# Kernel tuning notes

Measured on AMD Instinct MI355X. Metric: run time of the kernel, lower is better.

The kernel has to match this reference:

```python
import jax, jax.numpy as jnp
import numpy as np

VOCAB = 100000
EMB = 100
HID = 100
CTX_LEN = 60          # must equal MAX_DESC_LEN for linear_1 to fit
FACT_LEN = 20
DESC_LEN = 60


def setup_inputs() -> dict:
    key = jax.random.key(0)
    ks = jax.random.split(key, 12)
    s = 0.05
    context = jax.random.randint(ks[0], (CTX_LEN, FACT_LEN), 1, VOCAB)
    fact_lengths = jax.random.randint(ks[1], (CTX_LEN,), 1, FACT_LEN)
    description = jax.random.randint(ks[2], (DESC_LEN,), 1, VOCAB)
    emb_ctx = jax.random.normal(ks[3], (VOCAB, EMB), jnp.float32) * s
    emb_ctx = emb_ctx.at[0].set(0.0)  # padding_idx=0
    emb_dec = jax.random.normal(ks[4], (VOCAB, EMB), jnp.float32) * s
    emb_dec = emb_dec.at[0].set(0.0)
    w1 = jax.random.normal(ks[5], (HID, CTX_LEN * HID), jnp.float32) * s
    b1 = jax.random.normal(ks[6], (HID,), jnp.float32) * s
    w_ih = jax.random.normal(ks[7], (3 * HID, EMB), jnp.float32) * s
    w_hh = jax.random.normal(ks[8], (3 * HID, HID), jnp.float32) * s
    b_ih = jax.random.normal(ks[9], (3 * HID,), jnp.float32) * s
    b_hh = jax.random.normal(ks[10], (3 * HID,), jnp.float32) * s
    w_out = jax.random.normal(ks[11], (VOCAB, HID), jnp.float32) * s
    b_out = jnp.zeros((VOCAB,), jnp.float32)
    return {"context": context, "fact_lengths": fact_lengths, "description": description,
            "emb_ctx": emb_ctx, "emb_dec": emb_dec, "w1": w1, "b1": b1,
            "w_ih": w_ih, "w_hh": w_hh, "b_ih": b_ih, "b_hh": b_hh,
            "w_out": w_out, "b_out": b_out}


def _forward(context, description, emb_ctx, emb_dec, w1, b1,
             w_ih, w_hh, b_ih, b_hh, w_out, b_out):
    # ---- InputModule: embed + positional fact encoder ----
    emb = emb_ctx[context]                       # [CTX_LEN, FACT_LEN, EMB]
    slen, elen = FACT_LEN, EMB
    s = jnp.arange(slen, dtype=jnp.float32) / (slen - 1)   # [slen]
    e = jnp.arange(elen, dtype=jnp.float32) / (elen - 1)   # [elen]
    l = 1.0 - s[:, None] - e[None, :] * (1.0 - 2.0 * s[:, None])  # [slen, elen]
    facts = jnp.sum(emb * l[None], axis=1)       # [CTX_LEN, EMB]

    # ---- initial decoder hidden from flattened facts ----
    h0 = facts.reshape(1, -1) @ w1.T + b1        # [1, HID]

    x0 = emb_dec[1][None, :]                     # SOS token embedding [1, EMB]

    def step(carry, tok):
        h, x = carry
        gi = x @ w_ih.T + b_ih                   # [1, 3H]
        gh = h @ w_hh.T + b_hh
        i_r, i_z, i_n = jnp.split(gi, 3, axis=-1)
        h_r, h_z, h_n = jnp.split(gh, 3, axis=-1)
        r = jax.nn.sigmoid(i_r + h_r)
        z = jax.nn.sigmoid(i_z + h_z)
        n = jnp.tanh(i_n + r * h_n)
        h_new = (1.0 - z) * n + z * h            # [1, HID]
        logits = h_new @ w_out.T + b_out         # [1, VOCAB]
        logp = jax.nn.log_softmax(logits, axis=-1)
        loss_t = -logp[0, tok]                   # NLLLoss, batch 1
        x_next = emb_dec[tok][None, :]           # teacher forcing
        return (h_new, x_next), loss_t

    (_, _), losses = jax.lax.scan(step, (h0, x0), description)
    return jnp.sum(losses).reshape(1)            # matches torch FloatTensor([.])


def reference(context, fact_lengths, description, emb_ctx, emb_dec, w1, b1,
              w_ih, w_hh, b_ih, b_hh, w_out, b_out):
    # fact_lengths is unused by the original forward (PositionalFactEncoder ignores it)
    return _forward(context, description, emb_ctx, emb_dec, w1, b1,
                    w_ih, w_hh, b_ih, b_hh, w_out, b_out)
```

## Files before the change

### kernel.cpp

```cpp
#include <hip/hip_runtime.h>
#include <hip/hip_bf16.h>
#include <math.h>

#define VOCAB 100000
#define EMB 100
#define HID 100
#define CTX_LEN 60
#define FACT_LEN 20
#define DESC_LEN 60
#define NCHUNK (VOCAB / 16)

#define WS_FACTS 0
#define WS_X     6000
#define WS_H0    12000
#define WS_GI    12160
#define WS_H     30160
#define WS_MS    36864

typedef __attribute__((ext_vector_type(8))) short short8;
typedef __attribute__((ext_vector_type(4))) float f32x4;

static __device__ __forceinline__ unsigned short f2bf(float f) {
    union { float f; unsigned u; } x; x.f = f;
    unsigned r = (x.u + 0x7FFFu + ((x.u >> 16) & 1u)) >> 16;
    return (unsigned short)r;
}

__global__ __launch_bounds__(128) void k1_prep(const int* __restrict__ context,
                                               const int* __restrict__ desc,
                                               const float* __restrict__ emb_ctx,
                                               const float* __restrict__ emb_dec,
                                               float* __restrict__ ws,
                                               float* __restrict__ out) {
    int b = blockIdx.x, tid = threadIdx.x;
    if (b < 60) {
        __shared__ int toks[20];
        if (tid < 20) toks[tid] = context[b * 20 + tid];
        __syncthreads();
        if (tid < 100) {
            float ef = tid * (1.f / 99.f);
            float acc = 0.f;
            #pragma unroll
            for (int s = 0; s < 20; s++) {
                float sf = s * (1.f / 19.f);
                float l = 1.f - sf - ef * (1.f - 2.f * sf);
                acc = fmaf(emb_ctx[toks[s] * 100 + tid], l, acc);
            }
            ws[WS_FACTS + b * 100 + tid] = acc;
        }
    } else {
        int t = b - 60;
        int tok = (t == 0) ? 1 : desc[t - 1];
        if (tid < 100) ws[WS_X + t * 100 + tid] = emb_dec[tok * 100 + tid];
        if (b == 60 && tid == 0) out[0] = 0.f;
    }
}

__global__ __launch_bounds__(320) void k2_h0_gi(const float* __restrict__ w1,
                                                const float* __restrict__ b1,
                                                const float* __restrict__ w_ih,
                                                const float* __restrict__ b_ih,
                                                float* __restrict__ ws) {
    int b = blockIdx.x, tid = threadIdx.x;
    if (b < 100) {
        __shared__ float red[320];
        const float* facts = ws + WS_FACTS;
        const float* wr = w1 + b * 6000;
        float p = 0.f;
        for (int k = tid; k < 6000; k += 320) p = fmaf(facts[k], wr[k], p);
        red[tid] = p; __syncthreads();
        if (tid < 64) red[tid] += red[256 + tid];
        __syncthreads();
        for (int st = 128; st > 0; st >>= 1) {
            if (tid < st) red[tid] += red[tid + st];
            __syncthreads();
        }
        if (tid == 0) ws[WS_H0 + b] = red[0] + b1[b];
    } else {
        int t = b - 100;
        __shared__ float xs[100];
        if (tid < 100) xs[tid] = ws[WS_X + t * 100 + tid];
        __syncthreads();
        if (tid < 300) {
            float p = b_ih[tid];
            const float* wr = w_ih + tid * 100;
            #pragma unroll 4
            for (int k = 0; k < 100; k++) p = fmaf(wr[k], xs[k], p);
            ws[WS_GI + t * 300 + tid] = p;
        }
    }
}

__global__ __launch_bounds__(320, 1) void k3_gru(const float* __restrict__ w_hh,
                                                 const float* __restrict__ b_hh,
                                                 float* __restrict__ ws) {
    __shared__ __align__(16) float gi_lds[18000];
    __shared__ __align__(16) float h_hist[6000];
    __shared__ __align__(16) unsigned short h_bf[128];

    const int tid = threadIdx.x;
    const int wave = tid >> 6, lane = tid & 63;
    const int q = lane >> 4, n = lane & 15;
    const int l = lane;
    const int j = 20 * wave + l;

    short8 bfr[16];
    #pragma unroll
    for (int i = 0; i < 4; i++) {
        int row;
        if (i == 0)      row = 20 * wave + n;
        else if (i == 1) row = 100 + 20 * wave + n;
        else if (i == 2) row = 200 + 20 * wave + n;
        else {
            if (n < 4)       row = 20 * wave + 16 + n;
            else if (n < 8)  row = 100 + 20 * wave + 12 + n;
            else if (n < 12) row = 200 + 20 * wave + 8 + n;
            else             row = -1;
        }
        const float* wr = w_hh + (row < 0 ? 0 : row) * 100;
        #pragma unroll
        for (int kt = 0; kt < 4; kt++) {
            int k0 = kt * 32 + q * 8;
            float va[8];
            #pragma unroll
            for (int jj = 0; jj < 8; jj++) va[jj] = 0.f;
            if (row >= 0) {
                if (k0 + 4 <= 100) {
                    float4 a = *(const float4*)(wr + k0);
                    va[0] = a.x; va[1] = a.y; va[2] = a.z; va[3] = a.w;
                }
                if (k0 + 8 <= 100) {
                    float4 b = *(const float4*)(wr + k0 + 4);
                    va[4] = b.x; va[5] = b.y; va[6] = b.z; va[7] = b.w;
                }
            }
            short8 f;
            #pragma unroll
            for (int jj = 0; jj < 8; jj++) f[jj] = (short)f2bf(va[jj]);
            bfr[i * 4 + kt] = f;
        }
    }

    {
        const float4* g4 = (const float4*)(ws + WS_GI);
        float4* l4 = (float4*)gi_lds;
        for (int k = tid; k < 4500; k += 320) l4[k] = g4[k];
    }

    float hreg = 0.f, bh0 = 0.f, bh1 = 0.f, bh2 = 0.f;
    if (l < 20) {
        hreg = ws[WS_H0 + j];
        bh0 = b_hh[j]; bh1 = b_hh[100 + j]; bh2 = b_hh[200 + j];
        h_bf[j] = f2bf(hreg);
    }
    if (tid >= 100 && tid < 128) h_bf[tid] = 0;
    __syncthreads();

    const int s_lo  = (l < 16) ? l : 0;
    const int s3r   = (l < 16) ? 0 : (l - 16);
    const int s3z   = (l < 16) ? 4 : (l - 12);
    const int s3n   = (l < 16) ? 8 : (l - 8);

    for (int t = 0; t < 60; t++) {
        short8 afr[4];
        #pragma unroll
        for (int kt = 0; kt < 4; kt++)
            afr[kt] = *(const short8*)&h_bf[kt * 32 + q * 8];

        float val[4];
        #pragma unroll
        for (int i = 0; i < 4; i++) {
            f32x4 z4 = {0.f, 0.f, 0.f, 0.f};
            f32x4 a01 = __builtin_amdgcn_mfma_f32_16x16x32_bf16(afr[0], bfr[i * 4 + 0], z4, 0, 0, 0);
            a01 = __builtin_amdgcn_mfma_f32_16x16x32_bf16(afr[1], bfr[i * 4 + 1], a01, 0, 0, 0);
            f32x4 a23 = __builtin_amdgcn_mfma_f32_16x16x32_bf16(afr[2], bfr[i * 4 + 2], z4, 0, 0, 0);
            a23 = __builtin_amdgcn_mfma_f32_16x16x32_bf16(afr[3], bfr[i * 4 + 3], a23, 0, 0, 0);
            val[i] = a01[0] + a23[0];
        }

        float v0  = __shfl(val[0], s_lo, 64);
        float v1  = __shfl(val[1], s_lo, 64);
        float v2  = __shfl(val[2], s_lo, 64);
        float w3r = __shfl(val[3], s3r, 64);
        float w3z = __shfl(val[3], s3z, 64);
        float w3n = __shfl(val[3], s3n, 64);

        if (l < 20) {
            float ghr = ((l < 16) ? v0 : w3r) + bh0;
            float ghz = ((l < 16) ? v1 : w3z) + bh1;
            float ghn = ((l < 16) ? v2 : w3n) + bh2;
            float gir = gi_lds[t * 300 + j];
            float giz = gi_lds[t * 300 + 100 + j];
            float gin = gi_lds[t * 300 + 200 + j];
            float r = 1.f / (1.f + __expf(-(gir + ghr)));
            float z = 1.f / (1.f + __expf(-(giz + ghz)));
            float a = fmaf(r, ghn, gin);
            float tt = __expf(-2.f * fabsf(a));
            float nn = copysignf((1.f - tt) / (1.f + tt), a);
            hreg = (1.f - z) * nn + z * hreg;
            h_bf[j] = f2bf(hreg);
            h_hist[t * 100 + j] = hreg;
        }
        __syncthreads();
    }

    {
        float4* Hg = (float4*)(ws + WS_H);
        const float4* h4 = (const float4*)h_hist;
        for (int k = tid; k < 1500; k += 320) Hg[k] = h4[k];
    }
}

__global__ __launch_bounds__(256, 1) void k4_logits(const float* __restrict__ w_out,
                                                    const float* __restrict__ b_out,
                                                    float* __restrict__ ws,
                                                    int nwaves) {
    const float* H = ws + WS_H;
    float* ms = ws + WS_MS;
    const int lane = threadIdx.x & 63;
    const int gw = blockIdx.x * 4 + (threadIdx.x >> 6);
    const int q = lane >> 4, n = lane & 15;
    const int k_base = q * 8;

    short8 afr[4][4];
    #pragma unroll
    for (int mt = 0; mt < 4; mt++) {
        int m = mt * 16 + n;
        #pragma unroll
        for (int kt = 0; kt < 4; kt++) {
            int k0 = kt * 32 + k_base;
            float va[8];
            #pragma unroll
            for (int jj = 0; jj < 8; jj++) va[jj] = 0.f;
            if (m < 60) {
                if (k0 + 4 <= 100) {
                    float4 a = *(const float4*)(H + m * 100 + k0);
                    va[0] = a.x; va[1] = a.y; va[2] = a.z; va[3] = a.w;
                }
                if (k0 + 8 <= 100) {
                    float4 b = *(const float4*)(H + m * 100 + k0 + 4);
                    va[4] = b.x; va[5] = b.y; va[6] = b.z; va[7] = b.w;
                }
            }
            short8 f;
            #pragma unroll
            for (int jj = 0; jj < 8; jj++) f[jj] = (short)f2bf(va[jj]);
            afr[mt][kt] = f;
        }
    }

    float mS[16], sS[16];
    #pragma unroll
    for (int i = 0; i < 16; i++) { mS[i] = -3.0e38f; sS[i] = 0.f; }

    for (int c = gw; c < NCHUNK; c += nwaves) {
        int row = c * 16 + n;
        short8 bfr[4];
        #pragma unroll
        for (int kt = 0; kt < 4; kt++) {
            int k0 = kt * 32 + k_base;
            float va[8];
            #pragma unroll
            for (int jj = 0; jj < 8; jj++) va[jj] = 0.f;
            if (k0 + 4 <= 100) {
                float4 a = *(const float4*)(w_out + row * 100 + k0);
                va[0] = a.x; va[1] = a.y; va[2] = a.z; va[3] = a.w;
            }
            if (k0 + 8 <= 100) {
                float4 b = *(const float4*)(w_out + row * 100 + k0 + 4);
                va[4] = b.x; va[5] = b.y; va[6] = b.z; va[7] = b.w;
            }
            short8 f;
            #pragma unroll
            for (int jj = 0; jj < 8; jj++) f[jj] = (short)f2bf(va[jj]);
            bfr[kt] = f;
        }
        float bo = b_out[row];
        #pragma unroll
        for (int mt = 0; mt < 4; mt++) {
            f32x4 acc = {0.f, 0.f, 0.f, 0.f};
            acc = __builtin_amdgcn_mfma_f32_16x16x32_bf16(afr[mt][0], bfr[0], acc, 0, 0, 0);
            acc = __builtin_amdgcn_mfma_f32_16x16x32_bf16(afr[mt][1], bfr[1], acc, 0, 0, 0);
            acc = __builtin_amdgcn_mfma_f32_16x16x32_bf16(afr[mt][2], bfr[2], acc, 0, 0, 0);
            acc = __builtin_amdgcn_mfma_f32_16x16x32_bf16(afr[mt][3], bfr[3], acc, 0, 0, 0);
            #pragma unroll
            for (int reg = 0; reg < 4; reg++) {
                float x = acc[reg] + bo;
                int i = mt * 4 + reg;
                float mo = mS[i];
                float mn = fmaxf(mo, x);
                sS[i] = sS[i] * __expf(mo - mn) + __expf(x - mn);
                mS[i] = mn;
            }
        }
    }

    #pragma unroll
    for (int i = 0; i < 16; i++) {
        float m = mS[i], s = sS[i];
        #pragma unroll
        for (int off = 1; off < 16; off <<= 1) {
            float m2 = __shfl_xor(m, off);
            float s2 = __shfl_xor(s, off);
            float mn = fmaxf(m, m2);
            s = s * __expf(m - mn) + s2 * __expf(m2 - mn);
            m = mn;
        }
        mS[i] = m; sS[i] = s;
    }
    if (n == 0) {
        #pragma unroll
        for (int mt = 0; mt < 4; mt++) {
            #pragma unroll
            for (int reg = 0; reg < 4; reg++) {
                int t = mt * 16 + q * 4 + reg;
                int i = mt * 4 + reg;
                if (t < 60) {
                    float2 val; val.x = mS[i]; val.y = sS[i];
                    ((float2*)ms)[t * nwaves + gw] = val;
                }
            }
        }
    }
}

__global__ __launch_bounds__(256) void k5_final(const int* __restrict__ desc,
                                                const float* __restrict__ w_out,
                                                const float* __restrict__ b_out,
                                                const float* __restrict__ ws,
                                                float* __restrict__ out,
                                                int nwaves) {
    int t = blockIdx.x, tid = threadIdx.x;
    __shared__ float sm[256], ss[256], sd[256];
    const float2* ms = (const float2*)(ws + WS_MS);
    float m = -3.0e38f, s = 0.f;
    for (int i = tid; i < nwaves; i += 256) {
        float2 p = ms[t * nwaves + i];
        float mn = fmaxf(m, p.x);
        s = s * __expf(m - mn) + p.y * __expf(p.x - mn);
        m = mn;
    }
    sm[tid] = m; ss[tid] = s; __syncthreads();
    for (int st = 128; st > 0; st >>= 1) {
        if (tid < st) {
            float mo = sm[tid], so = ss[tid];
            float m2 = sm[tid + st], s2 = ss[tid + st];
            float mn = fmaxf(mo, m2);
            sm[tid] = mn;
            ss[tid] = so * __expf(mo - mn) + s2 * __expf(m2 - mn);
        }
        __syncthreads();
    }
    int tok = desc[t];
    float p = 0.f;
    if (tid < 100) p = ws[WS_H + t * 100 + tid] * w_out[tok * 100 + tid];
    sd[tid] = p; __syncthreads();
    for (int st = 128; st > 0; st >>= 1) {
        if (tid < st) sd[tid] += sd[tid + st];
        __syncthreads();
    }
    if (tid == 0) {
        float logit = sd[0] + b_out[tok];
        float loss = sm[0] + logf(ss[0]) - logit;
        atomicAdd(out, loss);
    }
}

extern "C" void kernel_launch(void* const* d_in, const int* in_sizes, int n_in,
                              void* d_out, int out_size, void* d_ws, size_t ws_size,
                              hipStream_t stream) {
    const int*   context = (const int*)d_in[0];
    const int*   desc    = (const int*)d_in[2];
    const float* emb_ctx = (const float*)d_in[3];
    const float* emb_dec = (const float*)d_in[4];
    const float* w1      = (const float*)d_in[5];
    const float* b1      = (const float*)d_in[6];
    const float* w_ih    = (const float*)d_in[7];
    const float* w_hh    = (const float*)d_in[8];
    const float* b_ih    = (const float*)d_in[9];
    const float* b_hh    = (const float*)d_in[10];
    const float* w_out   = (const float*)d_in[11];
    const float* b_out   = (const float*)d_in[12];
    float* out = (float*)d_out;
    float* ws  = (float*)d_ws;

    int nblocks = 1024;
    size_t need = (size_t)(WS_MS + 60 * (nblocks * 4) * 2) * 4;
    if (ws_size < need) nblocks = 256;
    int nwaves = nblocks * 4;

    k1_prep  <<<120, 128, 0, stream>>>(context, desc, emb_ctx, emb_dec, ws, out);
    k2_h0_gi <<<160, 320, 0, stream>>>(w1, b1, w_ih, b_ih, ws);
    k3_gru   <<<1,   320, 0, stream>>>(w_hh, b_hh, ws);
    k4_logits<<<nblocks, 256, 0, stream>>>(w_out, b_out, ws, nwaves);
    k5_final <<<60,  256, 0, stream>>>(desc, w_out, b_out, ws, out, nwaves);
}
```

Before: 214.4 us.

## Pre-convert w_out to padded bf16 in idle blocks alongside the serial GRU

The single-block GRU kernel is launched with 255 extra blocks that convert w_out from fp32 into a bf16 copy padded to 128 columns in the workspace. This uses the otherwise idle compute units during the serial recurrence. The logits kernel then loads ready-made bf16 fragments with plain vector loads, which removes the per-chunk conversion and reads fewer bytes. The cost is extra workspace traffic and memory that is written unconditionally, even when the workspace-size check falls back to fewer blocks. The extra blocks may also contend with the GRU block for memory bandwidth.

```diff
diff --git a/kernel.cpp b/kernel.cpp
--- a/kernel.cpp
+++ b/kernel.cpp
@@ -16,6 +16,7 @@
 #define WS_GI    12160
 #define WS_H     30160
 #define WS_MS    36864
+#define WS_WBF   1048576
 
 typedef __attribute__((ext_vector_type(8))) short short8;
 typedef __attribute__((ext_vector_type(4))) float f32x4;
@@ -91,9 +92,30 @@
     }
 }
 
-__global__ __launch_bounds__(320, 1) void k3_gru(const float* __restrict__ w_hh,
-                                                 const float* __restrict__ b_hh,
-                                                 float* __restrict__ ws) {
+__global__ __launch_bounds__(320, 1) void k3_gru_cvt(const float* __restrict__ w_hh,
+                                                     const float* __restrict__ b_hh,
+                                                     const float* __restrict__ w_out,
+                                                     float* __restrict__ ws) {
+    if (blockIdx.x != 0) {
+        const int bid = blockIdx.x - 1;
+        unsigned short* wbf = (unsigned short*)((char*)ws + WS_WBF * 4);
+        uint2* out4 = (uint2*)wbf;
+        const int total = VOCAB * 128 / 4;
+        const int stride = 255 * 320;
+        for (int i = bid * 320 + threadIdx.x; i < total; i += stride) {
+            int row = i >> 5;
+            int k0 = (i & 31) * 4;
+            uint2 r;
+            if (k0 + 4 <= 100) {
+                float4 v = *(const float4*)(w_out + row * 100 + k0);
+                r.x = (unsigned)f2bf(v.x) | ((unsigned)f2bf(v.y) << 16);
+                r.y = (unsigned)f2bf(v.z) | ((unsigned)f2bf(v.w) << 16);
+            } else { r.x = 0u; r.y = 0u; }
+            out4[i] = r;
+        }
+        return;
+    }
+
     __shared__ __align__(16) float gi_lds[18000];
     __shared__ __align__(16) float h_hist[6000];
     __shared__ __align__(16) unsigned short h_bf[128];
@@ -211,11 +233,11 @@
     }
 }
 
-__global__ __launch_bounds__(256, 1) void k4_logits(const float* __restrict__ w_out,
-                                                    const float* __restrict__ b_out,
+__global__ __launch_bounds__(256, 1) void k4_logits(const float* __restrict__ b_out,
                                                     float* __restrict__ ws,
                                                     int nwaves) {
     const float* H = ws + WS_H;
+    const unsigned short* wbf = (const unsigned short*)((const char*)ws + WS_WBF * 4);
     float* ms = ws + WS_MS;
     const int lane = threadIdx.x & 63;
     const int gw = blockIdx.x * 4 + (threadIdx.x >> 6);
@@ -255,26 +277,10 @@
 
     for (int c = gw; c < NCHUNK; c += nwaves) {
         int row = c * 16 + n;
+        const short8* bp = (const short8*)(wbf + (size_t)row * 128);
         short8 bfr[4];
         #pragma unroll
-        for (int kt = 0; kt < 4; kt++) {
-            int k0 = kt * 32 + k_base;
-            float va[8];
-            #pragma unroll
-            for (int jj = 0; jj < 8; jj++) va[jj] = 0.f;
-            if (k0 + 4 <= 100) {
-                float4 a = *(const float4*)(w_out + row * 100 + k0);
-                va[0] = a.x; va[1] = a.y; va[2] = a.z; va[3] = a.w;
-            }
-            if (k0 + 8 <= 100) {
-                float4 b = *(const float4*)(w_out + row * 100 + k0 + 4);
-                va[4] = b.x; va[5] = b.y; va[6] = b.z; va[7] = b.w;
-            }
-            short8 f;
-            #pragma unroll
-            for (int jj = 0; jj < 8; jj++) f[jj] = (short)f2bf(va[jj]);
-            bfr[kt] = f;
-        }
+        for (int kt = 0; kt < 4; kt++) bfr[kt] = bp[kt * 4 + q];
         float bo = b_out[row];
         #pragma unroll
         for (int mt = 0; mt < 4; mt++) {
@@ -385,13 +391,15 @@
     float* ws  = (float*)d_ws;
 
     int nblocks = 1024;
-    size_t need = (size_t)(WS_MS + 60 * (nblocks * 4) * 2) * 4;
+    size_t need = (size_t)(WS_WBF) * 4 + (size_t)VOCAB * 128 * 2;
+    size_t need_ms = (size_t)(WS_MS + 60 * (nblocks * 4) * 2) * 4;
+    if (need_ms > need) need = need_ms;
     if (ws_size < need) nblocks = 256;
     int nwaves = nblocks * 4;
 
-    k1_prep  <<<120, 128, 0, stream>>>(context, desc, emb_ctx, emb_dec, ws, out);
-    k2_h0_gi <<<160, 320, 0, stream>>>(w1, b1, w_ih, b_ih, ws);
-    k3_gru   <<<1,   320, 0, stream>>>(w_hh, b_hh, ws);
-    k4_logits<<<nblocks, 256, 0, stream>>>(w_out, b_out, ws, nwaves);
-    k5_final <<<60,  256, 0, stream>>>(desc, w_out, b_out, ws, out, nwaves);
-}
+    k1_prep   <<<120, 128, 0, stream>>>(context, desc, emb_ctx, emb_dec, ws, out);
+    k2_h0_gi  <<<160, 320, 0, stream>>>(w1, b1, w_ih, b_ih, ws);
+    k3_gru_cvt<<<256, 320, 0, stream>>>(w_hh, b_hh, w_out, ws);
+    k4_logits <<<nblocks, 256, 0, stream>>>(b_out, ws, nwaves);
+    k5_final  <<<60,  256, 0, stream>>>(desc, w_out, b_out, ws, out, nwaves);
+}
```

Result: no change. 211.5 us (-1.3%).

## Fuse fact encoding into h0 kernel and fix logits grid to 256 blocks

Applied to the files above, without the earlier changes.

Merges the prep and h0/input-gate kernels into one launch. Each h0 block now recomputes the positional fact encoding from embedding gathers, folded directly into its w1 dot product, and the decoder-input embedding is gathered inline in the gate blocks. This removes one kernel launch and the facts/x round-trip through the workspace, at the cost of redundant gathers and arithmetic in all 100 blocks. The logits kernel is also pinned to 256 blocks (1024 waves) as a compile-time constant, instead of picking 1024 blocks when the workspace allows. That gives each wave more vocab chunks and shrinks the partial-softmax reduction in the final kernel, in exchange for less parallelism in the logits GEMV.

```diff
diff --git a/kernel.cpp b/kernel.cpp
--- a/kernel.cpp
+++ b/kernel.cpp
@@ -9,9 +9,8 @@
 #define FACT_LEN 20
 #define DESC_LEN 60
 #define NCHUNK (VOCAB / 16)
-
-#define WS_FACTS 0
-#define WS_X     6000
+#define NWAVES 1024
+
 #define WS_H0    12000
 #define WS_GI    12160
 #define WS_H     30160
@@ -26,60 +25,57 @@
     return (unsigned short)r;
 }
 
-__global__ __launch_bounds__(128) void k1_prep(const int* __restrict__ context,
+__global__ __launch_bounds__(320) void k1_prep(const int* __restrict__ context,
                                                const int* __restrict__ desc,
                                                const float* __restrict__ emb_ctx,
                                                const float* __restrict__ emb_dec,
+                                               const float* __restrict__ w1,
+                                               const float* __restrict__ b1,
+                                               const float* __restrict__ w_ih,
+                                               const float* __restrict__ b_ih,
                                                float* __restrict__ ws,
                                                float* __restrict__ out) {
     int b = blockIdx.x, tid = threadIdx.x;
-    if (b < 60) {
-        __shared__ int toks[20];
-        if (tid < 20) toks[tid] = context[b * 20 + tid];
-        __syncthreads();
-        if (tid < 100) {
-            float ef = tid * (1.f / 99.f);
-            float acc = 0.f;
-            #pragma unroll
-            for (int s = 0; s < 20; s++) {
-                float sf = s * (1.f / 19.f);
-                float l = 1.f - sf - ef * (1.f - 2.f * sf);
-                acc = fmaf(emb_ctx[toks[s] * 100 + tid], l, acc);
-            }
-            ws[WS_FACTS + b * 100 + tid] = acc;
-        }
-    } else {
-        int t = b - 60;
-        int tok = (t == 0) ? 1 : desc[t - 1];
-        if (tid < 100) ws[WS_X + t * 100 + tid] = emb_dec[tok * 100 + tid];
-        if (b == 60 && tid == 0) out[0] = 0.f;
-    }
-}
-
-__global__ __launch_bounds__(320) void k2_h0_gi(const float* __restrict__ w1,
-                                                const float* __restrict__ b1,
-                                                const float* __restrict__ w_ih,
-                                                const float* __restrict__ b_ih,
-                                                float* __restrict__ ws) {
-    int b = blockIdx.x, tid = threadIdx.x;
     if (b < 100) {
+        __shared__ int toks[1200];
         __shared__ float red[320];
-        const float* facts = ws + WS_FACTS;
+        for (int i = tid; i < 1200; i += 320) toks[i] = context[i];
+        __syncthreads();
         const float* wr = w1 + b * 6000;
-        float p = 0.f;
-        for (int k = tid; k < 6000; k += 320) p = fmaf(facts[k], wr[k], p);
-        red[tid] = p; __syncthreads();
+        float acc = 0.f;
+        for (int p = tid; p < 1200; p += 320) {
+            int c = p / 20, s = p - c * 20;
+            const float* er = emb_ctx + (size_t)toks[p] * 100;
+            const float* wc = wr + c * 100;
+            float sf = s * (1.f / 19.f);
+            float l0 = 1.f - sf;
+            float l1 = 1.f - 2.f * sf;
+            float pacc = 0.f;
+            #pragma unroll 4
+            for (int e = 0; e < 100; e++) {
+                float l = fmaf(-(e * (1.f / 99.f)), l1, l0);
+                pacc = fmaf(er[e] * l, wc[e], pacc);
+            }
+            acc += pacc;
+        }
+        red[tid] = acc; __syncthreads();
         if (tid < 64) red[tid] += red[256 + tid];
         __syncthreads();
         for (int st = 128; st > 0; st >>= 1) {
             if (tid < st) red[tid] += red[tid + st];
             __syncthreads();
         }
-        if (tid == 0) ws[WS_H0 + b] = red[0] + b1[b];
+        if (tid == 0) {
+            ws[WS_H0 + b] = red[0] + b1[b];
+            if (b == 0) out[0] = 0.f;
+        }
     } else {
         int t = b - 100;
         __shared__ float xs[100];
-        if (tid < 100) xs[tid] = ws[WS_X + t * 100 + tid];
+        __shared__ int tok_s;
+        if (tid == 0) tok_s = (t == 0) ? 1 : desc[t - 1];
+        __syncthreads();
+        if (tid < 100) xs[tid] = emb_dec[tok_s * 100 + tid];
         __syncthreads();
         if (tid < 300) {
             float p = b_ih[tid];
@@ -213,8 +209,7 @@
 
 __global__ __launch_bounds__(256, 1) void k4_logits(const float* __restrict__ w_out,
                                                     const float* __restrict__ b_out,
-                                                    float* __restrict__ ws,
-                                                    int nwaves) {
+                                                    float* __restrict__ ws) {
     const float* H = ws + WS_H;
     float* ms = ws + WS_MS;
     const int lane = threadIdx.x & 63;
@@ -253,7 +248,7 @@
     #pragma unroll
     for (int i = 0; i < 16; i++) { mS[i] = -3.0e38f; sS[i] = 0.f; }
 
-    for (int c = gw; c < NCHUNK; c += nwaves) {
+    for (int c = gw; c < NCHUNK; c += NWAVES) {
         int row = c * 16 + n;
         short8 bfr[4];
         #pragma unroll
@@ -314,10 +309,10 @@
             #pragma unroll
             for (int reg = 0; reg < 4; reg++) {
                 int t = mt * 16 + q * 4 + reg;
-                int i = mt * 4 + reg;
                 if (t < 60) {
+                    int i = mt * 4 + reg;
                     float2 val; val.x = mS[i]; val.y = sS[i];
-                    ((float2*)ms)[t * nwaves + gw] = val;
+                    ((float2*)ms)[t * NWAVES + gw] = val;
                 }
             }
         }
@@ -328,14 +323,13 @@
                                                 const float* __restrict__ w_out,
                                                 const float* __restrict__ b_out,
                                                 const float* __restrict__ ws,
-                                                float* __restrict__ out,
-                                                int nwaves) {
+                                                float* __restrict__ out) {
     int t = blockIdx.x, tid = threadIdx.x;
     __shared__ float sm[256], ss[256], sd[256];
     const float2* ms = (const float2*)(ws + WS_MS);
     float m = -3.0e38f, s = 0.f;
-    for (int i = tid; i < nwaves; i += 256) {
-        float2 p = ms[t * nwaves + i];
+    for (int i = tid; i < NWAVES; i += 256) {
+        float2 p = ms[t * NWAVES + i];
         float mn = fmaxf(m, p.x);
         s = s * __expf(m - mn) + p.y * __expf(p.x - mn);
         m = mn;
@@ -384,14 +378,9 @@
     float* out = (float*)d_out;
     float* ws  = (float*)d_ws;
 
-    int nblocks = 1024;
-    size_t need = (size_t)(WS_MS + 60 * (nblocks * 4) * 2) * 4;
-    if (ws_size < need) nblocks = 256;
-    int nwaves = nblocks * 4;
-
-    k1_prep  <<<120, 128, 0, stream>>>(context, desc, emb_ctx, emb_dec, ws, out);
-    k2_h0_gi <<<160, 320, 0, stream>>>(w1, b1, w_ih, b_ih, ws);
+    k1_prep  <<<160, 320, 0, stream>>>(context, desc, emb_ctx, emb_dec,
+                                       w1, b1, w_ih, b_ih, ws, out);
     k3_gru   <<<1,   320, 0, stream>>>(w_hh, b_hh, ws);
-    k4_logits<<<nblocks, 256, 0, stream>>>(w_out, b_out, ws, nwaves);
-    k5_final <<<60,  256, 0, stream>>>(desc, w_out, b_out, ws, out, nwaves);
-}
+    k4_logits<<<256, 256, 0, stream>>>(w_out, b_out, ws);
+    k5_final <<<60,  256, 0, stream>>>(desc, w_out, b_out, ws, out);
+}
```

Result: slower. 245.5 us (+14.5%).

## Stage w_out chunks through LDS with coalesced loads and register prefetch

Applied to the files above, without the earlier changes.

The logits kernel now loads each wave's 16-row w_out chunk as contiguous float4s, converts them to bf16 and writes them into a per-wave double-buffered LDS tile. The MFMA B fragments are then read back from LDS. The next chunk is prefetched into registers while the current one is consumed, which is meant to replace strided, partly masked global loads with coalesced streaming and to overlap memory with compute. The grid is fixed at 256 blocks (1024 waves) and the workspace-size fallback is removed. This adds LDS traffic, register pressure from the prefetch buffers, and a risk that the workspace is too small.

```diff
diff --git a/kernel.cpp b/kernel.cpp
--- a/kernel.cpp
+++ b/kernel.cpp
@@ -9,6 +9,7 @@
 #define FACT_LEN 20
 #define DESC_LEN 60
 #define NCHUNK (VOCAB / 16)
+#define NWAVES 1024
 
 #define WS_FACTS 0
 #define WS_X     6000
@@ -213,14 +214,21 @@
 
 __global__ __launch_bounds__(256, 1) void k4_logits(const float* __restrict__ w_out,
                                                     const float* __restrict__ b_out,
-                                                    float* __restrict__ ws,
-                                                    int nwaves) {
+                                                    float* __restrict__ ws) {
+    __shared__ __align__(16) unsigned short stg[4][2][16 * 136];
     const float* H = ws + WS_H;
     float* ms = ws + WS_MS;
-    const int lane = threadIdx.x & 63;
-    const int gw = blockIdx.x * 4 + (threadIdx.x >> 6);
+    const int tid = threadIdx.x;
+    const int wave = tid >> 6, lane = tid & 63;
+    const int gw = blockIdx.x * 4 + wave;
     const int q = lane >> 4, n = lane & 15;
     const int k_base = q * 8;
+
+    for (int i = lane; i < 16 * 36; i += 64) {
+        int r = i / 36, c = 100 + (i % 36);
+        stg[wave][0][r * 136 + c] = 0;
+        stg[wave][1][r * 136 + c] = 0;
+    }
 
     short8 afr[4][4];
     #pragma unroll
@@ -253,29 +261,52 @@
     #pragma unroll
     for (int i = 0; i < 16; i++) { mS[i] = -3.0e38f; sS[i] = 0.f; }
 
-    for (int c = gw; c < NCHUNK; c += nwaves) {
-        int row = c * 16 + n;
+    float4 pf[7];
+    const int f_lane = lane * 4;
+    {
+        const float* src = w_out + (size_t)gw * 1600;
+        #pragma unroll
+        for (int r = 0; r < 7; r++) {
+            int f = r * 256 + f_lane;
+            if (f < 1600) pf[r] = *(const float4*)(src + f);
+        }
+    }
+
+    int iter = 0;
+    for (int c = gw; c < NCHUNK; c += NWAVES, iter++) {
+        const int buf = iter & 1;
+        {
+            unsigned short* dst = stg[wave][buf];
+            #pragma unroll
+            for (int r = 0; r < 7; r++) {
+                int f = r * 256 + f_lane;
+                if (f < 1600) {
+                    int row = f / 100;
+                    int col = f - row * 100;
+                    uint2 v;
+                    v.x = (unsigned)f2bf(pf[r].x) | ((unsigned)f2bf(pf[r].y) << 16);
+                    v.y = (unsigned)f2bf(pf[r].z) | ((unsigned)f2bf(pf[r].w) << 16);
+                    *(uint2*)(dst + row * 136 + col) = v;
+                }
+            }
+        }
+        {
+            int cn = c + NWAVES;
+            if (cn < NCHUNK) {
+                const float* src = w_out + (size_t)cn * 1600;
+                #pragma unroll
+                for (int r = 0; r < 7; r++) {
+                    int f = r * 256 + f_lane;
+                    if (f < 1600) pf[r] = *(const float4*)(src + f);
+                }
+            }
+        }
+        const unsigned short* base = stg[wave][buf] + n * 136;
         short8 bfr[4];
         #pragma unroll
-        for (int kt = 0; kt < 4; kt++) {
-            int k0 = kt * 32 + k_base;
-            float va[8];
-            #pragma unroll
-            for (int jj = 0; jj < 8; jj++) va[jj] = 0.f;
-            if (k0 + 4 <= 100) {
-                float4 a = *(const float4*)(w_out + row * 100 + k0);
-                va[0] = a.x; va[1] = a.y; va[2] = a.z; va[3] = a.w;
-            }
-            if (k0 + 8 <= 100) {
-                float4 b = *(const float4*)(w_out + row * 100 + k0 + 4);
-                va[4] = b.x; va[5] = b.y; va[6] = b.z; va[7] = b.w;
-            }
-            short8 f;
-            #pragma unroll
-            for (int jj = 0; jj < 8; jj++) f[jj] = (short)f2bf(va[jj]);
-            bfr[kt] = f;
-        }
-        float bo = b_out[row];
+        for (int kt = 0; kt < 4; kt++)
+            bfr[kt] = *(const short8*)(base + kt * 32 + k_base);
+        float bo = b_out[c * 16 + n];
         #pragma unroll
         for (int mt = 0; mt < 4; mt++) {
             f32x4 acc = {0.f, 0.f, 0.f, 0.f};
@@ -314,10 +345,10 @@
             #pragma unroll
             for (int reg = 0; reg < 4; reg++) {
                 int t = mt * 16 + q * 4 + reg;
-                int i = mt * 4 + reg;
                 if (t < 60) {
+                    int i = mt * 4 + reg;
                     float2 val; val.x = mS[i]; val.y = sS[i];
-                    ((float2*)ms)[t * nwaves + gw] = val;
+                    ((float2*)ms)[t * NWAVES + gw] = val;
                 }
             }
         }
@@ -328,14 +359,13 @@
                                                 const float* __restrict__ w_out,
                                                 const float* __restrict__ b_out,
                                                 const float* __restrict__ ws,
-                                                float* __restrict__ out,
-                                                int nwaves) {
+                                                float* __restrict__ out) {
     int t = blockIdx.x, tid = threadIdx.x;
     __shared__ float sm[256], ss[256], sd[256];
     const float2* ms = (const float2*)(ws + WS_MS);
     float m = -3.0e38f, s = 0.f;
-    for (int i = tid; i < nwaves; i += 256) {
-        float2 p = ms[t * nwaves + i];
+    for (int i = tid; i < NWAVES; i += 256) {
+        float2 p = ms[t * NWAVES + i];
         float mn = fmaxf(m, p.x);
         s = s * __expf(m - mn) + p.y * __expf(p.x - mn);
         m = mn;
@@ -384,14 +414,9 @@
     float* out = (float*)d_out;
     float* ws  = (float*)d_ws;
 
-    int nblocks = 1024;
-    size_t need = (size_t)(WS_MS + 60 * (nblocks * 4) * 2) * 4;
-    if (ws_size < need) nblocks = 256;
-    int nwaves = nblocks * 4;
-
     k1_prep  <<<120, 128, 0, stream>>>(context, desc, emb_ctx, emb_dec, ws, out);
     k2_h0_gi <<<160, 320, 0, stream>>>(w1, b1, w_ih, b_ih, ws);
     k3_gru   <<<1,   320, 0, stream>>>(w_hh, b_hh, ws);
-    k4_logits<<<nblocks, 256, 0, stream>>>(w_out, b_out, ws, nwaves);
-    k5_final <<<60,  256, 0, stream>>>(desc, w_out, b_out, ws, out, nwaves);
-}
+    k4_logits<<<256, 256, 0, stream>>>(w_out, b_out, ws);
+    k5_final <<<60,  256, 0, stream>>>(desc, w_out, b_out, ws, out);
+}
```

Result: faster. 204.7 us (-4.5%).
